# Kernel optimization log

Measured on AMD Instinct MI355X. Metric: run time of the kernel, lower is better.

Reference implementation:

```python
import jax, jax.numpy as jnp
import numpy as np
from jax import lax

B, P_IN, C_IN = 32, 2048, 256
STAGES = [(512, 256, 16), (256, 256, 16)]  # (P_out, C_out, K)
EPS = 1e-5


def _bn(x, g, b):
    # BatchNorm in training-mode forward: batch stats over all dims but channel (axis 1)
    ax = (0,) + tuple(range(2, x.ndim))
    m = x.mean(ax, keepdims=True)
    v = x.var(ax, keepdims=True)
    sh = (1, -1) + (1,) * (x.ndim - 2)
    return (x - m) * lax.rsqrt(v + EPS) * g.reshape(sh) + b.reshape(sh)


def _fps(coords, valid, n_out):
    # coords (2,P), valid (P,) bool -> (n_out,) int32 indices of farthest points
    start = jnp.argmax(valid)
    dist0 = jnp.where(valid, jnp.inf, -jnp.inf)

    def step(carry, _):
        dist, last = carry
        d = jnp.sum((coords - coords[:, last][:, None]) ** 2, axis=0)
        dist = jnp.where(valid, jnp.minimum(dist, d), -jnp.inf)
        return (dist, jnp.argmax(dist)), last

    _, idx = lax.scan(step, (dist0, start), None, length=n_out)
    return idx


def _stage(coords, feats, mask, p_out, k, w1, g1, b1, w2, g2, b2, wsc, gsc, bsc):
    idx = jax.vmap(_fps, (0, 0, None))(coords, mask[:, 0, :], p_out)       # (B,Pout)
    cc = jnp.take_along_axis(coords, idx[:, None, :], axis=2)              # (B,2,Pout)
    cf = jnp.take_along_axis(feats, idx[:, None, :], axis=2)               # (B,C,Pout)
    # kNN of centroids against all input points, invalid points pushed to +inf
    d = jnp.sum((cc[:, :, :, None] - coords[:, :, None, :]) ** 2, axis=1)  # (B,Pout,P)
    d = jnp.where(mask[:, 0, None, :], d, jnp.inf)
    nidx = lax.top_k(-d, k)[1]                                             # (B,Pout,K)
    nf = jnp.take_along_axis(feats[:, :, None, :], nidx[:, None, :, :], axis=3)  # (B,C,Pout,K)
    nm = jnp.take_along_axis(mask[:, :, None, :].astype(feats.dtype), nidx[:, None, :, :], axis=3)
    x = jnp.concatenate([jnp.broadcast_to(cf[..., None], nf.shape), nf], axis=1)  # (B,2C,Pout,K)
    h = jax.nn.relu(_bn(jnp.einsum('oc,bcpk->bopk', w1, x), g1, b1))
    h = _bn(jnp.einsum('oc,bcpk->bopk', w2, h), g2, b2)
    msg = jnp.where(nm > 0, h, -jnp.inf)
    pooled = msg.max(axis=-1)                                              # (B,Cout,Pout)
    pooled = jnp.where(jnp.isfinite(pooled), pooled, 0.0)                  # nan_to_num + -inf fill
    sc = _bn(jnp.einsum('oc,bcp->bop', wsc, cf), gsc, bsc)
    out = jax.nn.relu(pooled + sc)
    return cc, out, jnp.ones((coords.shape[0], 1, p_out), bool)


def setup_inputs() -> dict:
    key = jax.random.key(0)
    ks = jax.random.split(key, 32)
    inp = {
        'coordinates': jax.random.normal(ks[0], (B, 2, P_IN), jnp.float32),
        'features': jax.random.normal(ks[1], (B, C_IN, P_IN), jnp.float32),
        'mask': jnp.ones((B, 1, P_IN), bool),
    }
    cin = C_IN
    ki = 2
    for i, (_, cout, _) in enumerate(STAGES):
        s = f's{i + 1}_'
        inp[s + 'w1'] = jax.random.normal(ks[ki], (cout, 2 * cin), jnp.float32) / np.float32(np.sqrt(2 * cin)); ki += 1
        inp[s + 'g1'] = jnp.ones(cout, jnp.float32); inp[s + 'b1'] = jnp.zeros(cout, jnp.float32)
        inp[s + 'w2'] = jax.random.normal(ks[ki], (cout, cout), jnp.float32) / np.float32(np.sqrt(cout)); ki += 1
        inp[s + 'g2'] = jnp.ones(cout, jnp.float32); inp[s + 'b2'] = jnp.zeros(cout, jnp.float32)
        inp[s + 'wsc'] = jax.random.normal(ks[ki], (cout, cin), jnp.float32) / np.float32(np.sqrt(cin)); ki += 1
        inp[s + 'gsc'] = jnp.ones(cout, jnp.float32); inp[s + 'bsc'] = jnp.zeros(cout, jnp.float32)
        cin = cout
    return inp


def reference(coordinates, features, mask,
              s1_w1, s1_g1, s1_b1, s1_w2, s1_g2, s1_b2, s1_wsc, s1_gsc, s1_bsc,
              s2_w1, s2_g1, s2_b1, s2_w2, s2_g2, s2_b2, s2_wsc, s2_gsc, s2_bsc):
    c, f, m = coordinates, features, mask
    c, f, m = _stage(c, f, m, STAGES[0][0], STAGES[0][2],
                     s1_w1, s1_g1, s1_b1, s1_w2, s1_g2, s1_b2, s1_wsc, s1_gsc, s1_bsc)
    c, f, m = _stage(c, f, m, STAGES[1][0], STAGES[1][2],
                     s2_w1, s2_g1, s2_b1, s2_w2, s2_g2, s2_b2, s2_wsc, s2_gsc, s2_bsc)
    return f, c, m
```

## Files before the change

### kernel.cpp

```cpp
#include <hip/hip_runtime.h>
#include <hip/hip_bf16.h>


#define DEVI __device__ __forceinline__

typedef __attribute__((ext_vector_type(8))) short bf16x8;
typedef __attribute__((ext_vector_type(4))) float f32x4;

constexpr int B_   = 32;
constexpr int P1   = 2048;
constexpr int PO1  = 512;
constexpr int PO2  = 256;
constexpr int KNN  = 16;
constexpr float EPS_ = 1e-5f;

constexpr size_t OFF_FB1   = 0;
constexpr size_t SZ_FB1    = (size_t)B_ * P1 * 256 * 2;
constexpr size_t OFF_FB2   = OFF_FB1 + SZ_FB1;
constexpr size_t SZ_FB2    = (size_t)B_ * PO1 * 256 * 2;
constexpr size_t OFF_H     = OFF_FB2 + SZ_FB2;
constexpr size_t SZ_H      = (size_t)B_ * PO1 * KNN * 256 * 2;
constexpr size_t OFF_POOL  = OFF_H + SZ_H;
constexpr size_t SZ_POOL   = (size_t)B_ * PO1 * 256 * 4;
constexpr size_t OFF_SC    = OFF_POOL + SZ_POOL;
constexpr size_t SZ_SC     = SZ_POOL;
constexpr size_t OFF_CC1   = OFF_SC + SZ_SC;
constexpr size_t SZ_CC1    = (size_t)B_ * 2 * PO1 * 4;
constexpr size_t OFF_IDX1  = OFF_CC1 + SZ_CC1;
constexpr size_t OFF_IDX2  = OFF_IDX1 + (size_t)B_ * PO1 * 4;
constexpr size_t OFF_NIDX1 = OFF_IDX2 + (size_t)B_ * PO2 * 4;
constexpr size_t OFF_NIDX2 = OFF_NIDX1 + (size_t)B_ * PO1 * KNN * 4;
constexpr size_t OFF_STATS = OFF_NIDX2 + (size_t)B_ * PO2 * KNN * 4;
constexpr size_t OFF_BNAB  = OFF_STATS + 12 * 256 * 4;
constexpr size_t OFF_WB    = OFF_BNAB + 12 * 256 * 4;
constexpr size_t OFF_W1B1  = OFF_WB;
constexpr size_t OFF_W2B1  = OFF_W1B1 + 262144;
constexpr size_t OFF_WSB1  = OFF_W2B1 + 131072;
constexpr size_t OFF_W1B2  = OFF_WSB1 + 131072;
constexpr size_t OFF_W2B2  = OFF_W1B2 + 262144;
constexpr size_t OFF_WSB2  = OFF_W2B2 + 131072;

DEVI unsigned int pack2bf(float a, float b) {
    __hip_bfloat16 ha = __float2bfloat16(a), hb = __float2bfloat16(b);
    unsigned short ua, ub;
    __builtin_memcpy(&ua, &ha, 2);
    __builtin_memcpy(&ub, &hb, 2);
    return (unsigned int)ua | ((unsigned int)ub << 16);
}
DEVI unsigned short f2bf(float f) {
    __hip_bfloat16 h = __float2bfloat16(f);
    unsigned short u;
    __builtin_memcpy(&u, &h, 2);
    return u;
}

DEVI void gload_lds16(const void* g, void* l) {
    __builtin_amdgcn_global_load_lds(
        (const __attribute__((address_space(1))) unsigned int*)g,
        (__attribute__((address_space(3))) unsigned int*)l, 16, 0, 0);
}

__global__ __launch_bounds__(256) void transpose_bf16(const float* __restrict__ in,
                                                      unsigned short* __restrict__ out) {
    __shared__ float tile[32][33];
    const int b = blockIdx.z, p0 = blockIdx.x * 32, c0 = blockIdx.y * 32;
    const int tx = threadIdx.x & 31, ty = threadIdx.x >> 5;
#pragma unroll
    for (int k2 = 0; k2 < 4; ++k2)
        tile[ty + k2 * 8][tx] = in[((size_t)b * 256 + c0 + ty + k2 * 8) * P1 + p0 + tx];
    __syncthreads();
#pragma unroll
    for (int it = 0; it < 2; ++it) {
        const int id = threadIdx.x + it * 256;
        const int pl = id >> 4, u = id & 15;
        const unsigned int v = pack2bf(tile[2 * u][pl], tile[2 * u + 1][pl]);
        *(unsigned int*)&out[((size_t)b * P1 + p0 + pl) * 256 + c0 + 2 * u] = v;
    }
}

__global__ void cvt_bf16(const float* __restrict__ in, unsigned short* __restrict__ out,
                         int n4) {
    const int i = blockIdx.x * 256 + threadIdx.x;
    if (i < n4) {
        const float4 f = ((const float4*)in)[i];
        uint2 o;
        o.x = pack2bf(f.x, f.y);
        o.y = pack2bf(f.z, f.w);
        ((uint2*)out)[i] = o;
    }
}

template <int P_, int POUT_>
DEVI void fps_core(const float* __restrict__ coords, int* __restrict__ idx,
                   int t, int b, float2* cxy ) {
    const int lane = t & 63;
    constexpr int E = P_ / 64;
    const float* cb = coords + (size_t)b * 2 * P_;
    float xs[E], ys[E], dist[E];
    if (t < 64) {
#pragma unroll
        for (int i = 0; i < E; ++i) {
            const int p = i * 64 + lane;
            xs[i] = cb[p];
            ys[i] = cb[P_ + p];
            dist[i] = __builtin_inff();
            float2 v;
            v.x = xs[i];
            v.y = ys[i];
            cxy[p] = v;
        }
    }
    __syncthreads();
    if (t >= 64) return;
    int last = 0;
    int* ob = idx + b * POUT_;
    for (int it = 0; it < POUT_; ++it) {
        if (lane == 0) ob[it] = last;
        const float2 lc = cxy[last];
        float bv = -__builtin_inff();
        int bi = 0;
#pragma unroll
        for (int i = 0; i < E; ++i) {
            const float dx = xs[i] - lc.x, dy = ys[i] - lc.y;
            const float d = dx * dx + dy * dy;
            const float nd = fminf(dist[i], d);
            dist[i] = nd;
            if (nd > bv) { bv = nd; bi = i * 64 + lane; }
        }
#pragma unroll
        for (int off = 1; off < 64; off <<= 1) {
            const float ov = __shfl_xor(bv, off);
            const int oi = __shfl_xor(bi, off);
            if (ov > bv || (ov == bv && oi < bi)) { bv = ov; bi = oi; }
        }
        last = bi;
    }
}

template <int P_, int POUT_>
__global__ __launch_bounds__(64) void fps_wave(const float* __restrict__ coords,
                                               int* __restrict__ idx) {
    __shared__ float2 cxy[P_];
    fps_core<P_, POUT_>(coords, idx, threadIdx.x, blockIdx.x, cxy);
}

template <int P_, int POUT_>
DEVI void knn_core(const float* __restrict__ coords, const int* __restrict__ idx,
                   int* __restrict__ nidx, float* __restrict__ cc,
                   int t, int bid, float* xs, float* ys) {
    constexpr int BPB = POUT_ / 4;
    const int b = bid / BPB;
    const int j = (bid % BPB) * 4 + (t >> 6);
    const int lane = t & 63;
    const float* cb = coords + (size_t)b * 2 * P_;
    for (int i = t; i < P_; i += 256) { xs[i] = cb[i]; ys[i] = cb[P_ + i]; }
    __syncthreads();
    const int cidx = idx[b * POUT_ + j];
    const float cx = xs[cidx], cy = ys[cidx];
    constexpr int LPT = P_ / 64;
    float dl[LPT];
#pragma unroll
    for (int i = 0; i < LPT; ++i) {
        const int p = i * 64 + lane;
        const float dx = xs[p] - cx, dy = ys[p] - cy;
        dl[i] = dx * dx + dy * dy;
    }
    int* ob = nidx + ((size_t)b * POUT_ + j) * KNN;
    for (int it = 0; it < KNN; ++it) {
        float bv = __builtin_inff();
        int bi = 0x7fffffff;
#pragma unroll
        for (int i = 0; i < LPT; ++i)
            if (dl[i] < bv) { bv = dl[i]; bi = i * 64 + lane; }
#pragma unroll
        for (int off = 1; off < 64; off <<= 1) {
            const float ov = __shfl_xor(bv, off);
            const int oi = __shfl_xor(bi, off);
            if (ov < bv || (ov == bv && oi < bi)) { bv = ov; bi = oi; }
        }
        const bool win = (lane == (bi & 63));
        const int slot = bi >> 6;
#pragma unroll
        for (int i = 0; i < LPT; ++i)
            if (win && i == slot) dl[i] = __builtin_inff();
        if (lane == 0) ob[it] = bi;
    }
    if (lane == 0) {
        cc[((size_t)b * 2 + 0) * POUT_ + j] = cx;
        cc[((size_t)b * 2 + 1) * POUT_ + j] = cy;
    }
}

template <int P_, int POUT_>
__global__ __launch_bounds__(256) void knn_kernel(const float* __restrict__ coords,
                                                  const int* __restrict__ idx,
                                                  int* __restrict__ nidx,
                                                  float* __restrict__ cc) {
    __shared__ float xs[P_], ys[P_];
    knn_core<P_, POUT_>(coords, idx, nidx, cc, threadIdx.x, blockIdx.x, xs, ys);
}

template <int MODE, int KTOT, int POUT_, int P_, bool FUSE_FPS, int FPS_P, int FPS_POUT>
__global__ __launch_bounds__(256) void gemm_mfma(
    const unsigned short* __restrict__ Abase,
    const unsigned short* __restrict__ Wb,
    const int* __restrict__ idx,
    const int* __restrict__ nidx,
    unsigned short* __restrict__ hout,
    float* __restrict__ pooled,
    float* __restrict__ scout,
    float* __restrict__ ssum, float* __restrict__ ssq,
    const float* __restrict__ fpsC, int* __restrict__ fpsIdx) {
    __shared__ unsigned short As[128 * 64];
    __shared__ unsigned short Bs[128 * 64];
    if constexpr (FUSE_FPS) {
        if (blockIdx.x < 32) {
            fps_core<FPS_P, FPS_POUT>(fpsC, fpsIdx, threadIdx.x, blockIdx.x,
                                      (float2*)As);
            return;
        }
    }
    const int fid = FUSE_FPS ? (int)blockIdx.x - 32 : (int)blockIdx.x;
    const int n0 = (fid >> 1) * 128, c0 = (fid & 1) * 128;
    const int t = threadIdx.x;
    const int w = t >> 6, lane = t & 63;
    const int wr = w >> 1, wc = w & 1;
    const int col16 = lane & 15, kg = lane >> 4;
    const int srow8 = lane >> 3;
    const int scho = ((lane & 7) ^ srow8) * 16;
    constexpr int LP = (POUT_ == 512) ? 9 : 8;

    const char* aSrc0[4];
    const char* aSrc1[4];
    const char* bSrc[4];
#pragma unroll
    for (int i = 0; i < 4; ++i) {
        const int rA = w * 32 + i * 8 + srow8;
        if constexpr (MODE == 0) {
            const int n = n0 + rA, bp = n >> 4, b = bp >> LP;
            aSrc0[i] = (const char*)(Abase + ((size_t)b * P_ + idx[bp]) * 256) + scho;
            aSrc1[i] = (const char*)(Abase + ((size_t)b * P_ + nidx[n]) * 256) + scho;
        } else if constexpr (MODE == 1) {
            aSrc0[i] = (const char*)(Abase + (size_t)(n0 + rA) * 256) + scho;
            aSrc1[i] = nullptr;
        } else {
            const int n = n0 + rA, b = n >> LP;
            aSrc0[i] = (const char*)(Abase + ((size_t)b * P_ + idx[n]) * 256) + scho;
            aSrc1[i] = nullptr;
        }
        bSrc[i] = (const char*)(Wb + (size_t)(c0 + rA) * KTOT) + scho;
    }

    f32x4 acc[4][4];
#pragma unroll
    for (int m = 0; m < 4; ++m)
#pragma unroll
        for (int n = 0; n < 4; ++n) acc[m][n] = {0.f, 0.f, 0.f, 0.f};

    for (int kt = 0; kt < KTOT; kt += 64) {
#pragma unroll
        for (int i = 0; i < 4; ++i) {
            const char* ga;
            if constexpr (MODE == 0)
                ga = (kt < 256 ? aSrc0[i] : aSrc1[i]) + (size_t)(kt & 255) * 2;
            else
                ga = aSrc0[i] + (size_t)kt * 2;
            gload_lds16(ga, (char*)As + (w * 4 + i) * 1024);
            gload_lds16(bSrc[i] + (size_t)kt * 2, (char*)Bs + (w * 4 + i) * 1024);
        }
        __syncthreads();
#pragma unroll
        for (int ks = 0; ks < 2; ++ks) {
            bf16x8 af[4], bfr[4];
#pragma unroll
            for (int m = 0; m < 4; ++m) {
                const int row = wr * 64 + m * 16 + col16;
                const int off = row * 64 + ((((ks << 2) | kg) ^ (col16 & 7)) << 3);
                af[m] = *(const bf16x8*)&As[off];
            }
#pragma unroll
            for (int n = 0; n < 4; ++n) {
                const int row = wc * 64 + n * 16 + col16;
                const int off = row * 64 + ((((ks << 2) | kg) ^ (col16 & 7)) << 3);
                bfr[n] = *(const bf16x8*)&Bs[off];
            }
#pragma unroll
            for (int m = 0; m < 4; ++m)
#pragma unroll
                for (int n = 0; n < 4; ++n)
                    acc[m][n] = __builtin_amdgcn_mfma_f32_16x16x32_bf16(
                        af[m], bfr[n], acc[m][n], 0, 0, 0);
        }
        __syncthreads();
    }

    const int orow0 = n0 + wr * 64 + kg * 4;
    const int ocol = c0 + wc * 64 + col16;
    if constexpr (MODE == 0) {
#pragma unroll
        for (int m = 0; m < 4; ++m)
#pragma unroll
            for (int n = 0; n < 4; ++n)
#pragma unroll
                for (int r = 0; r < 4; ++r)
                    hout[(size_t)(orow0 + m * 16 + r) * 256 + ocol + n * 16] =
                        f2bf(acc[m][n][r]);
    } else if constexpr (MODE == 1) {
#pragma unroll
        for (int m = 0; m < 4; ++m) {
            const int bp = (n0 >> 4) + wr * 4 + m;
#pragma unroll
            for (int n = 0; n < 4; ++n) {
                float mx = fmaxf(fmaxf(acc[m][n][0], acc[m][n][1]),
                                 fmaxf(acc[m][n][2], acc[m][n][3]));
                mx = fmaxf(mx, __shfl_xor(mx, 16));
                mx = fmaxf(mx, __shfl_xor(mx, 32));
                if (lane < 16)
                    pooled[(size_t)bp * 256 + c0 + wc * 64 + n * 16 + lane] = mx;
            }
        }
    } else {
#pragma unroll
        for (int m = 0; m < 4; ++m)
#pragma unroll
            for (int n = 0; n < 4; ++n)
#pragma unroll
                for (int r = 0; r < 4; ++r)
                    scout[(size_t)(orow0 + m * 16 + r) * 256 + ocol + n * 16] =
                        acc[m][n][r];
    }

    float s4[4], q4[4];
#pragma unroll
    for (int n = 0; n < 4; ++n) {
        float s = 0.f, q = 0.f;
#pragma unroll
        for (int m = 0; m < 4; ++m)
#pragma unroll
            for (int r = 0; r < 4; ++r) {
                const float v = acc[m][n][r];
                s += v;
                q += v * v;
            }
        s += __shfl_xor(s, 16);
        s += __shfl_xor(s, 32);
        q += __shfl_xor(q, 16);
        q += __shfl_xor(q, 32);
        s4[n] = s;
        q4[n] = q;
    }
    float* red = (float*)As;
    __syncthreads();
    if (lane < 16) {
#pragma unroll
        for (int n = 0; n < 4; ++n) {
            red[w * 64 + n * 16 + lane] = s4[n];
            red[256 + w * 64 + n * 16 + lane] = q4[n];
        }
    }
    __syncthreads();
    if (t < 128) {
        const int c = t;
        const float sv = red[(c >> 6) * 64 + (c & 63)] + red[128 + (c >> 6) * 64 + (c & 63)];
        atomicAdd(ssum + c0 + c, sv);
    } else if (t < 256) {
        const int c = t - 128;
        const float qv =
            red[256 + (c >> 6) * 64 + (c & 63)] + red[384 + (c >> 6) * 64 + (c & 63)];
        atomicAdd(ssq + c0 + c, qv);
    }
}

DEVI void bnrelu_body(unsigned short* __restrict__ h, const float* sA, const float* sB,
                      int i0, int stride, int n8) {
    for (int i = i0; i < n8; i += stride) {
        uint4 raw = ((const uint4*)h)[i];
        const int cb = (i * 8) & 255;
        float v[8];
        v[0] = __uint_as_float((raw.x & 0xffffu) << 16);
        v[1] = __uint_as_float(raw.x & 0xffff0000u);
        v[2] = __uint_as_float((raw.y & 0xffffu) << 16);
        v[3] = __uint_as_float(raw.y & 0xffff0000u);
        v[4] = __uint_as_float((raw.z & 0xffffu) << 16);
        v[5] = __uint_as_float(raw.z & 0xffff0000u);
        v[6] = __uint_as_float((raw.w & 0xffffu) << 16);
        v[7] = __uint_as_float(raw.w & 0xffff0000u);
#pragma unroll
        for (int j = 0; j < 8; ++j) v[j] = fmaxf(0.f, fmaf(v[j], sA[cb + j], sB[cb + j]));
        uint4 o;
        o.x = pack2bf(v[0], v[1]);
        o.y = pack2bf(v[2], v[3]);
        o.z = pack2bf(v[4], v[5]);
        o.w = pack2bf(v[6], v[7]);
        ((uint4*)h)[i] = o;
    }
}

__global__ __launch_bounds__(256) void bnrelu_h(unsigned short* __restrict__ h,
                                                const float* __restrict__ A,
                                                const float* __restrict__ Bb,
                                                int n8) {
    __shared__ float sA[256], sB[256];
    sA[threadIdx.x] = A[threadIdx.x];
    sB[threadIdx.x] = Bb[threadIdx.x];
    __syncthreads();
    bnrelu_body(h, sA, sB, blockIdx.x * 256 + threadIdx.x, gridDim.x * 256, n8);
}

__global__ __launch_bounds__(256) void bnrelu_knn2(
    unsigned short* __restrict__ h, const float* __restrict__ A,
    const float* __restrict__ Bb,
    const float* __restrict__ cc1, const int* __restrict__ idx2,
    int* __restrict__ nidx2, float* __restrict__ ccout) {
    __shared__ float xs[PO1], ys[PO1];
    __shared__ float sA[256], sB[256];
    const int t = threadIdx.x;
    if (blockIdx.x < 2048) {
        knn_core<PO1, PO2>(cc1, idx2, nidx2, ccout, t, blockIdx.x, xs, ys);
        return;
    }
    sA[t] = A[t];
    sB[t] = Bb[t];
    __syncthreads();
    bnrelu_body(h, sA, sB, ((int)blockIdx.x - 2048) * 256 + t, 2048 * 256, 8388608);
}

__global__ void bn_finalize(const float* __restrict__ ssum, const float* __restrict__ ssq,
                            const float* __restrict__ g, const float* __restrict__ bb,
                            float invN, float* __restrict__ A, float* __restrict__ Bo) {
    const int c = threadIdx.x;
    const float m = ssum[c] * invN;
    const float v = ssq[c] * invN - m * m;
    const float a = g[c] * rsqrtf(v + EPS_);
    A[c] = a;
    Bo[c] = bb[c] - m * a;
}

__global__ __launch_bounds__(256) void finalize1(const float* __restrict__ pool,
                                                 const float* __restrict__ sc,
                                                 const float* __restrict__ A2,
                                                 const float* __restrict__ B2,
                                                 const float* __restrict__ Asc,
                                                 const float* __restrict__ Bsc,
                                                 unsigned short* __restrict__ outT) {
    const size_t e = ((size_t)blockIdx.x * 256 + threadIdx.x) * 4;
    const int c = (int)(e & 255);
    const float4 p = *(const float4*)(pool + e);
    const float4 s = *(const float4*)(sc + e);
    float o0 = fmaxf(0.f, p.x * A2[c + 0] + B2[c + 0] + s.x * Asc[c + 0] + Bsc[c + 0]);
    float o1 = fmaxf(0.f, p.y * A2[c + 1] + B2[c + 1] + s.y * Asc[c + 1] + Bsc[c + 1]);
    float o2 = fmaxf(0.f, p.z * A2[c + 2] + B2[c + 2] + s.z * Asc[c + 2] + Bsc[c + 2]);
    float o3 = fmaxf(0.f, p.w * A2[c + 3] + B2[c + 3] + s.w * Asc[c + 3] + Bsc[c + 3]);
    uint2 o;
    o.x = pack2bf(o0, o1);
    o.y = pack2bf(o2, o3);
    *(uint2*)&outT[e] = o;
}

__global__ __launch_bounds__(256) void finalize2(const float* __restrict__ pool,
                                                 const float* __restrict__ sc,
                                                 const float* __restrict__ A2,
                                                 const float* __restrict__ B2,
                                                 const float* __restrict__ Asc,
                                                 const float* __restrict__ Bsc,
                                                 float* __restrict__ out) {
    __shared__ float tile[32][33];
    const int b = blockIdx.z, p0 = blockIdx.x * 32, c0 = blockIdx.y * 32;
    const int tx = threadIdx.x & 31, ty = threadIdx.x >> 5;
#pragma unroll
    for (int k2 = 0; k2 < 4; ++k2) {
        const int p = p0 + ty + k2 * 8;
        const int c = c0 + tx;
        const size_t e = ((size_t)b * 256 + p) * 256 + c;
        tile[ty + k2 * 8][tx] =
            fmaxf(0.f, pool[e] * A2[c] + B2[c] + sc[e] * Asc[c] + Bsc[c]);
    }
    __syncthreads();
#pragma unroll
    for (int k2 = 0; k2 < 4; ++k2) {
        const int c = c0 + ty + k2 * 8;
        out[((size_t)b * 256 + c) * 256 + p0 + tx] = tile[tx][ty + k2 * 8];
    }
}

__global__ void ones_kernel(float* __restrict__ p) {
    p[blockIdx.x * 256 + threadIdx.x] = 1.0f;
}

extern "C" void kernel_launch(void* const* d_in, const int* in_sizes, int n_in,
                              void* d_out, int out_size, void* d_ws, size_t ws_size,
                              hipStream_t stream) {
    (void)in_sizes; (void)n_in; (void)out_size; (void)ws_size;
    const float* coords = (const float*)d_in[0];
    const float* feats  = (const float*)d_in[1];
    const float* w1_1  = (const float*)d_in[3];
    const float* g1_1  = (const float*)d_in[4];
    const float* b1_1  = (const float*)d_in[5];
    const float* w2_1  = (const float*)d_in[6];
    const float* g2_1  = (const float*)d_in[7];
    const float* b2_1  = (const float*)d_in[8];
    const float* wsc_1 = (const float*)d_in[9];
    const float* gsc_1 = (const float*)d_in[10];
    const float* bsc_1 = (const float*)d_in[11];
    const float* w1_2  = (const float*)d_in[12];
    const float* g1_2  = (const float*)d_in[13];
    const float* b1_2  = (const float*)d_in[14];
    const float* w2_2  = (const float*)d_in[15];
    const float* g2_2  = (const float*)d_in[16];
    const float* b2_2  = (const float*)d_in[17];
    const float* wsc_2 = (const float*)d_in[18];
    const float* gsc_2 = (const float*)d_in[19];
    const float* bsc_2 = (const float*)d_in[20];

    char* ws = (char*)d_ws;
    unsigned short* fb1 = (unsigned short*)(ws + OFF_FB1);
    unsigned short* fb2 = (unsigned short*)(ws + OFF_FB2);
    unsigned short* hbuf = (unsigned short*)(ws + OFF_H);
    float* pool = (float*)(ws + OFF_POOL);
    float* scb  = (float*)(ws + OFF_SC);
    float* cc1  = (float*)(ws + OFF_CC1);
    int* idx1   = (int*)(ws + OFF_IDX1);
    int* idx2   = (int*)(ws + OFF_IDX2);
    int* nidx1  = (int*)(ws + OFF_NIDX1);
    int* nidx2  = (int*)(ws + OFF_NIDX2);
    float* S    = (float*)(ws + OFF_STATS);
    float* AB   = (float*)(ws + OFF_BNAB);
    unsigned short* w1b1 = (unsigned short*)(ws + OFF_W1B1);
    unsigned short* w2b1 = (unsigned short*)(ws + OFF_W2B1);
    unsigned short* wsb1 = (unsigned short*)(ws + OFF_WSB1);
    unsigned short* w1b2 = (unsigned short*)(ws + OFF_W1B2);
    unsigned short* w2b2 = (unsigned short*)(ws + OFF_W2B2);
    unsigned short* wsb2 = (unsigned short*)(ws + OFF_WSB2);

    float* fout  = (float*)d_out;
    float* ccout = fout + (size_t)B_ * 256 * 256;
    float* mout  = ccout + (size_t)B_ * 2 * 256;

    hipMemsetAsync(ws + OFF_STATS, 0, 12 * 256 * 4, stream);

    cvt_bf16<<<128, 256, 0, stream>>>(w1_1, w1b1, 32768);
    cvt_bf16<<<64, 256, 0, stream>>>(w2_1, w2b1, 16384);
    cvt_bf16<<<64, 256, 0, stream>>>(wsc_1, wsb1, 16384);
    cvt_bf16<<<128, 256, 0, stream>>>(w1_2, w1b2, 32768);
    cvt_bf16<<<64, 256, 0, stream>>>(w2_2, w2b2, 16384);
    cvt_bf16<<<64, 256, 0, stream>>>(wsc_2, wsb2, 16384);

    transpose_bf16<<<dim3(64, 8, 32), 256, 0, stream>>>(feats, fb1);
    fps_wave<P1, PO1><<<B_, 64, 0, stream>>>(coords, idx1);
    knn_kernel<P1, PO1><<<B_ * (PO1 / 4), 256, 0, stream>>>(coords, idx1, nidx1, cc1);
    gemm_mfma<0, 512, PO1, P1, true, PO1, PO2><<<32 + 4096, 256, 0, stream>>>(
        fb1, w1b1, idx1, nidx1, hbuf, nullptr, nullptr, S + 0 * 256, S + 1 * 256,
        cc1, idx2);
    bn_finalize<<<1, 256, 0, stream>>>(S + 0 * 256, S + 1 * 256, g1_1, b1_1,
                                       1.f / (B_ * PO1 * KNN), AB + 0 * 256, AB + 1 * 256);
    bnrelu_knn2<<<4096, 256, 0, stream>>>(hbuf, AB + 0 * 256, AB + 1 * 256,
                                          cc1, idx2, nidx2, ccout);
    gemm_mfma<1, 256, PO1, P1, false, 64, 1><<<4096, 256, 0, stream>>>(
        hbuf, w2b1, nullptr, nullptr, nullptr, pool, nullptr, S + 2 * 256, S + 3 * 256,
        nullptr, nullptr);
    gemm_mfma<2, 256, PO1, P1, false, 64, 1><<<256, 256, 0, stream>>>(
        fb1, wsb1, idx1, nullptr, nullptr, nullptr, scb, S + 4 * 256, S + 5 * 256,
        nullptr, nullptr);
    bn_finalize<<<1, 256, 0, stream>>>(S + 2 * 256, S + 3 * 256, g2_1, b2_1,
                                       1.f / (B_ * PO1 * KNN), AB + 2 * 256, AB + 3 * 256);
    bn_finalize<<<1, 256, 0, stream>>>(S + 4 * 256, S + 5 * 256, gsc_1, bsc_1,
                                       1.f / (B_ * PO1), AB + 4 * 256, AB + 5 * 256);
    finalize1<<<(B_ * PO1 * 256) / 1024, 256, 0, stream>>>(
        pool, scb, AB + 2 * 256, AB + 3 * 256, AB + 4 * 256, AB + 5 * 256, fb2);

    gemm_mfma<0, 512, PO2, PO1, false, 64, 1><<<2048, 256, 0, stream>>>(
        fb2, w1b2, idx2, nidx2, hbuf, nullptr, nullptr, S + 6 * 256, S + 7 * 256,
        nullptr, nullptr);
    bn_finalize<<<1, 256, 0, stream>>>(S + 6 * 256, S + 7 * 256, g1_2, b1_2,
                                       1.f / (B_ * PO2 * KNN), AB + 6 * 256, AB + 7 * 256);
    bnrelu_h<<<2048, 256, 0, stream>>>(hbuf, AB + 6 * 256, AB + 7 * 256, 4194304);
    gemm_mfma<1, 256, PO2, PO1, false, 64, 1><<<2048, 256, 0, stream>>>(
        hbuf, w2b2, nullptr, nullptr, nullptr, pool, nullptr, S + 8 * 256, S + 9 * 256,
        nullptr, nullptr);
    gemm_mfma<2, 256, PO2, PO1, false, 64, 1><<<128, 256, 0, stream>>>(
        fb2, wsb2, idx2, nullptr, nullptr, nullptr, scb, S + 10 * 256, S + 11 * 256,
        nullptr, nullptr);
    bn_finalize<<<1, 256, 0, stream>>>(S + 8 * 256, S + 9 * 256, g2_2, b2_2,
                                       1.f / (B_ * PO2 * KNN), AB + 8 * 256, AB + 9 * 256);
    bn_finalize<<<1, 256, 0, stream>>>(S + 10 * 256, S + 11 * 256, gsc_2, bsc_2,
                                       1.f / (B_ * PO2), AB + 10 * 256, AB + 11 * 256);
    finalize2<<<dim3(8, 8, 32), 256, 0, stream>>>(
        pool, scb, AB + 8 * 256, AB + 9 * 256, AB + 10 * 256, AB + 11 * 256, fout);
    ones_kernel<<<B_, 256, 0, stream>>>(mout);
}
```

Measured before the change: 1.274 ms.

## Fuse FPS, transpose and weight casts into one front kernel; DPP reductions

The six weight-conversion launches, the feature transpose and stage-1 FPS are merged into one front_kernel. The FPS blocks come first so they overlap with the bandwidth-bound transpose and cast blocks. FPS now carries the winning point's coordinates through a DPP-based argmax with four independent partial maxima instead of a shuffle-xor reduction plus an LDS lookup. kNN top-k selection also uses a DPP argmin followed by readlane. These changes cut launch count and the latency of the serial FPS loop, at the cost of more registers and 256-thread blocks in which only one wave does the FPS work.

New measurement: 1.335 ms. 4.8% more time.

```diff
diff --git a/kernel.cpp b/kernel.cpp
--- a/kernel.cpp
+++ b/kernel.cpp
@@ -60,27 +60,113 @@
         (__attribute__((address_space(3))) unsigned int*)l, 16, 0, 0);
 }
 
-__global__ __launch_bounds__(256) void transpose_bf16(const float* __restrict__ in,
-                                                      unsigned short* __restrict__ out) {
-    __shared__ float tile[32][33];
-    const int b = blockIdx.z, p0 = blockIdx.x * 32, c0 = blockIdx.y * 32;
-    const int tx = threadIdx.x & 31, ty = threadIdx.x >> 5;
+template <int CTRL, int RMASK>
+DEVI void argmax_step(float& v, int& i, float& x, float& y) {
+    const float nv = __int_as_float(__builtin_amdgcn_update_dpp(
+        __float_as_int(v), __float_as_int(v), CTRL, RMASK, 0xf, false));
+    const int ni = __builtin_amdgcn_update_dpp(i, i, CTRL, RMASK, 0xf, false);
+    const float nx = __int_as_float(__builtin_amdgcn_update_dpp(
+        __float_as_int(x), __float_as_int(x), CTRL, RMASK, 0xf, false));
+    const float ny = __int_as_float(__builtin_amdgcn_update_dpp(
+        __float_as_int(y), __float_as_int(y), CTRL, RMASK, 0xf, false));
+    const bool tk = (nv > v) || (nv == v && ni < i);
+    v = tk ? nv : v;
+    i = tk ? ni : i;
+    x = tk ? nx : x;
+    y = tk ? ny : y;
+}
+template <int CTRL, int RMASK>
+DEVI void argmin_step(float& v, int& i) {
+    const float nv = __int_as_float(__builtin_amdgcn_update_dpp(
+        __float_as_int(v), __float_as_int(v), CTRL, RMASK, 0xf, false));
+    const int ni = __builtin_amdgcn_update_dpp(i, i, CTRL, RMASK, 0xf, false);
+    const bool tk = (nv < v) || (nv == v && ni < i);
+    v = tk ? nv : v;
+    i = tk ? ni : i;
+}
+
+template <int P_, int POUT_>
+DEVI void fps_core(const float* __restrict__ coords, int* __restrict__ idx,
+                   int t, int b) {
+    if (t >= 64) return;
+    const int lane = t;
+    constexpr int E = P_ / 64;
+    const float* cb = coords + (size_t)b * 2 * P_;
+    float xs[E], ys[E], dist[E];
+#pragma unroll
+    for (int i = 0; i < E; ++i) {
+        xs[i] = cb[i * 64 + lane];
+        ys[i] = cb[P_ + i * 64 + lane];
+        dist[i] = __builtin_inff();
+    }
+    float lx = cb[0], ly = cb[P_];
+    int last = 0;
+    int* ob = idx + b * POUT_;
+    for (int it = 0; it < POUT_; ++it) {
+        if (lane == 0) ob[it] = last;
+        float bv[4], bx[4], by[4];
+        int bi[4];
+#pragma unroll
+        for (int j = 0; j < 4; ++j) {
+            bv[j] = -__builtin_inff();
+            bi[j] = 0;
+            bx[j] = 0.f;
+            by[j] = 0.f;
+        }
+#pragma unroll
+        for (int i = 0; i < E; ++i) {
+            const int j = i & 3;
+            const float dx = xs[i] - lx, dy = ys[i] - ly;
+            const float d = dx * dx + dy * dy;
+            const float nd = fminf(dist[i], d);
+            dist[i] = nd;
+            const bool tk = nd > bv[j];
+            bv[j] = tk ? nd : bv[j];
+            bi[j] = tk ? i * 64 + lane : bi[j];
+            bx[j] = tk ? xs[i] : bx[j];
+            by[j] = tk ? ys[i] : by[j];
+        }
+#pragma unroll
+        for (int j = 1; j < 4; ++j) {
+            const bool tk = (bv[j] > bv[0]) || (bv[j] == bv[0] && bi[j] < bi[0]);
+            bv[0] = tk ? bv[j] : bv[0];
+            bi[0] = tk ? bi[j] : bi[0];
+            bx[0] = tk ? bx[j] : bx[0];
+            by[0] = tk ? by[j] : by[0];
+        }
+        float v = bv[0], x = bx[0], y = by[0];
+        int ii = bi[0];
+        argmax_step<0x111, 0xf>(v, ii, x, y);
+        argmax_step<0x112, 0xf>(v, ii, x, y);
+        argmax_step<0x114, 0xf>(v, ii, x, y);
+        argmax_step<0x118, 0xf>(v, ii, x, y);
+        argmax_step<0x142, 0xa>(v, ii, x, y);
+        argmax_step<0x143, 0xc>(v, ii, x, y);
+        last = __builtin_amdgcn_readlane(ii, 63);
+        lx = __int_as_float(__builtin_amdgcn_readlane(__float_as_int(x), 63));
+        ly = __int_as_float(__builtin_amdgcn_readlane(__float_as_int(y), 63));
+    }
+}
+
+DEVI void transpose_body(const float* __restrict__ in, unsigned short* __restrict__ out,
+                         int bx, int by, int bz, float (*tile)[33], int t) {
+    const int p0 = bx * 32, c0 = by * 32, b = bz;
+    const int tx = t & 31, ty = t >> 5;
 #pragma unroll
     for (int k2 = 0; k2 < 4; ++k2)
         tile[ty + k2 * 8][tx] = in[((size_t)b * 256 + c0 + ty + k2 * 8) * P1 + p0 + tx];
     __syncthreads();
 #pragma unroll
     for (int it = 0; it < 2; ++it) {
-        const int id = threadIdx.x + it * 256;
+        const int id = t + it * 256;
         const int pl = id >> 4, u = id & 15;
         const unsigned int v = pack2bf(tile[2 * u][pl], tile[2 * u + 1][pl]);
         *(unsigned int*)&out[((size_t)b * P1 + p0 + pl) * 256 + c0 + 2 * u] = v;
     }
 }
 
-__global__ void cvt_bf16(const float* __restrict__ in, unsigned short* __restrict__ out,
-                         int n4) {
-    const int i = blockIdx.x * 256 + threadIdx.x;
+DEVI void cvt_body(const float* __restrict__ in, unsigned short* __restrict__ out,
+                   int i, int n4) {
     if (i < n4) {
         const float4 f = ((const float4*)in)[i];
         uint2 o;
@@ -90,58 +176,38 @@
     }
 }
 
-template <int P_, int POUT_>
-DEVI void fps_core(const float* __restrict__ coords, int* __restrict__ idx,
-                   int t, int b, float2* cxy ) {
-    const int lane = t & 63;
-    constexpr int E = P_ / 64;
-    const float* cb = coords + (size_t)b * 2 * P_;
-    float xs[E], ys[E], dist[E];
-    if (t < 64) {
-#pragma unroll
-        for (int i = 0; i < E; ++i) {
-            const int p = i * 64 + lane;
-            xs[i] = cb[p];
-            ys[i] = cb[P_ + p];
-            dist[i] = __builtin_inff();
-            float2 v;
-            v.x = xs[i];
-            v.y = ys[i];
-            cxy[p] = v;
-        }
-    }
-    __syncthreads();
-    if (t >= 64) return;
-    int last = 0;
-    int* ob = idx + b * POUT_;
-    for (int it = 0; it < POUT_; ++it) {
-        if (lane == 0) ob[it] = last;
-        const float2 lc = cxy[last];
-        float bv = -__builtin_inff();
-        int bi = 0;
-#pragma unroll
-        for (int i = 0; i < E; ++i) {
-            const float dx = xs[i] - lc.x, dy = ys[i] - lc.y;
-            const float d = dx * dx + dy * dy;
-            const float nd = fminf(dist[i], d);
-            dist[i] = nd;
-            if (nd > bv) { bv = nd; bi = i * 64 + lane; }
-        }
-#pragma unroll
-        for (int off = 1; off < 64; off <<= 1) {
-            const float ov = __shfl_xor(bv, off);
-            const int oi = __shfl_xor(bi, off);
-            if (ov > bv || (ov == bv && oi < bi)) { bv = ov; bi = oi; }
-        }
-        last = bi;
-    }
-}
-
-template <int P_, int POUT_>
-__global__ __launch_bounds__(64) void fps_wave(const float* __restrict__ coords,
-                                               int* __restrict__ idx) {
-    __shared__ float2 cxy[P_];
-    fps_core<P_, POUT_>(coords, idx, threadIdx.x, blockIdx.x, cxy);
+__global__ __launch_bounds__(256, 1) void front_kernel(
+    const float* __restrict__ coords, int* __restrict__ idx1,
+    const float* __restrict__ feats, unsigned short* __restrict__ fb1,
+    const float* __restrict__ w1_1, unsigned short* __restrict__ w1b1,
+    const float* __restrict__ w2_1, unsigned short* __restrict__ w2b1,
+    const float* __restrict__ wsc_1, unsigned short* __restrict__ wsb1,
+    const float* __restrict__ w1_2, unsigned short* __restrict__ w1b2,
+    const float* __restrict__ w2_2, unsigned short* __restrict__ w2b2,
+    const float* __restrict__ wsc_2, unsigned short* __restrict__ wsb2) {
+    __shared__ float tile[32][33];
+    const int bid = blockIdx.x;
+    const int t = threadIdx.x;
+    if (bid < 32) {
+        fps_core<P1, PO1>(coords, idx1, t, bid);
+        return;
+    }
+    if (bid < 32 + 16384) {
+        const int b2 = bid - 32;
+        transpose_body(feats, fb1, b2 & 63, (b2 >> 6) & 7, b2 >> 9, tile, t);
+        return;
+    }
+    const int id = bid - 16416;
+    const float* src;
+    unsigned short* dst;
+    int lid, n4;
+    if (id < 128)      { src = w1_1;  dst = w1b1; lid = id;       n4 = 32768; }
+    else if (id < 192) { src = w2_1;  dst = w2b1; lid = id - 128; n4 = 16384; }
+    else if (id < 256) { src = wsc_1; dst = wsb1; lid = id - 192; n4 = 16384; }
+    else if (id < 384) { src = w1_2;  dst = w1b2; lid = id - 256; n4 = 32768; }
+    else if (id < 448) { src = w2_2;  dst = w2b2; lid = id - 384; n4 = 16384; }
+    else               { src = wsc_2; dst = wsb2; lid = id - 448; n4 = 16384; }
+    cvt_body(src, dst, lid * 256 + t, n4);
 }
 
 template <int P_, int POUT_>
@@ -170,20 +236,24 @@
         float bv = __builtin_inff();
         int bi = 0x7fffffff;
 #pragma unroll
-        for (int i = 0; i < LPT; ++i)
-            if (dl[i] < bv) { bv = dl[i]; bi = i * 64 + lane; }
-#pragma unroll
-        for (int off = 1; off < 64; off <<= 1) {
-            const float ov = __shfl_xor(bv, off);
-            const int oi = __shfl_xor(bi, off);
-            if (ov < bv || (ov == bv && oi < bi)) { bv = ov; bi = oi; }
-        }
-        const bool win = (lane == (bi & 63));
-        const int slot = bi >> 6;
+        for (int i = 0; i < LPT; ++i) {
+            const bool tk = dl[i] < bv;
+            bv = tk ? dl[i] : bv;
+            bi = tk ? i * 64 + lane : bi;
+        }
+        argmin_step<0x111, 0xf>(bv, bi);
+        argmin_step<0x112, 0xf>(bv, bi);
+        argmin_step<0x114, 0xf>(bv, bi);
+        argmin_step<0x118, 0xf>(bv, bi);
+        argmin_step<0x142, 0xa>(bv, bi);
+        argmin_step<0x143, 0xc>(bv, bi);
+        const int g = __builtin_amdgcn_readlane(bi, 63);
+        const bool win = (lane == (g & 63));
+        const int slot = g >> 6;
 #pragma unroll
         for (int i = 0; i < LPT; ++i)
             if (win && i == slot) dl[i] = __builtin_inff();
-        if (lane == 0) ob[it] = bi;
+        if (lane == 0) ob[it] = g;
     }
     if (lane == 0) {
         cc[((size_t)b * 2 + 0) * POUT_ + j] = cx;
@@ -215,8 +285,7 @@
     __shared__ unsigned short Bs[128 * 64];
     if constexpr (FUSE_FPS) {
         if (blockIdx.x < 32) {
-            fps_core<FPS_P, FPS_POUT>(fpsC, fpsIdx, threadIdx.x, blockIdx.x,
-                                      (float2*)As);
+            fps_core<FPS_P, FPS_POUT>(fpsC, fpsIdx, threadIdx.x, blockIdx.x);
             return;
         }
     }
@@ -538,15 +607,10 @@
 
     hipMemsetAsync(ws + OFF_STATS, 0, 12 * 256 * 4, stream);
 
-    cvt_bf16<<<128, 256, 0, stream>>>(w1_1, w1b1, 32768);
-    cvt_bf16<<<64, 256, 0, stream>>>(w2_1, w2b1, 16384);
-    cvt_bf16<<<64, 256, 0, stream>>>(wsc_1, wsb1, 16384);
-    cvt_bf16<<<128, 256, 0, stream>>>(w1_2, w1b2, 32768);
-    cvt_bf16<<<64, 256, 0, stream>>>(w2_2, w2b2, 16384);
-    cvt_bf16<<<64, 256, 0, stream>>>(wsc_2, wsb2, 16384);
-
-    transpose_bf16<<<dim3(64, 8, 32), 256, 0, stream>>>(feats, fb1);
-    fps_wave<P1, PO1><<<B_, 64, 0, stream>>>(coords, idx1);
+    front_kernel<<<32 + 16384 + 512, 256, 0, stream>>>(
+        coords, idx1, feats, fb1, w1_1, w1b1, w2_1, w2b1, wsc_1, wsb1,
+        w1_2, w1b2, w2_2, w2b2, wsc_2, wsb2);
+
     knn_kernel<P1, PO1><<<B_ * (PO1 / 4), 256, 0, stream>>>(coords, idx1, nidx1, cc1);
     gemm_mfma<0, 512, PO1, P1, true, PO1, PO2><<<32 + 4096, 256, 0, stream>>>(
         fb1, w1b1, idx1, nidx1, hbuf, nullptr, nullptr, S + 0 * 256, S + 1 * 256,
```
